# Performance work log

Hardware: AMD Instinct MI355X
Metric: run time of the kernel (lower is better)

Reference implementation:

```python
import jax, jax.numpy as jnp
import numpy as np

B, D, R, W, K = 1024, 256, 16384, 64, 3


def setup_inputs() -> dict:
    key = jax.random.key(0)
    ks = jax.random.split(key, 8)
    s = lambda k, shape: jax.random.normal(k, shape, jnp.float32) * 0.05
    return {
        'x': jax.random.normal(ks[0], (B, D), jnp.float32),
        'Wv': s(ks[1], (D, W)), 'bv': jnp.zeros((W,), jnp.float32),
        'Wb': s(ks[2], (D, 1)), 'bb': jnp.zeros((1,), jnp.float32),
        'Wg': s(ks[3], (D, 1)), 'bg': jnp.zeros((1,), jnp.float32),
        'Wp': s(ks[4], (D, R)), 'bp': jnp.zeros((R,), jnp.float32),
        # positive conv weights keep the pre-sharpening address non-negative,
        # so address ** gamma is well defined (as in a trained NTM shift kernel)
        'conv_k': jax.random.uniform(ks[5], (K, 1, 1), jnp.float32),
        'conv_b': jnp.zeros((1,), jnp.float32),
        'mem': jax.random.normal(ks[6], (R, W), jnp.float32),
    }


def reference(x, Wv, bv, Wb, bb, Wg, bg, Wp, bp, conv_k, conv_b, mem):
    eps = 1e-16
    # controller heads
    v = x @ Wv + bv                                  # [B, W] writing value (key)
    beta = jax.nn.softplus(x @ Wb + bb)              # [B, 1] key strength
    gamma = 1.0 + jax.nn.softplus(x @ Wg + bg)       # [B, 1] sharpening
    # content addressing: cosine similarity against memory rows
    vn = jnp.linalg.norm(v, axis=-1, keepdims=True)  # [B, 1]
    mn = jnp.linalg.norm(mem, axis=-1, keepdims=True)  # [R, 1]
    sim = (v @ mem.T) / (vn * mn.T + eps)            # [B, R]
    w = jax.nn.softmax(beta * sim, axis=-1)          # [B, R]
    # circular-ish shift via Conv1D('same') over the mem_rows axis
    wc = jax.lax.conv_general_dilated(
        w[..., None], conv_k, (1,), 'SAME',
        dimension_numbers=('NWC', 'WIO', 'NWC')) + conv_b  # [B, R, 1]
    a = wc[..., 0] ** gamma                          # sharpen
    a = a / jnp.sum(a + eps, axis=1, keepdims=True)  # renormalize (matches tf sum(a+eps))
    # memory write (batch-averaged erase-free additive write, shared memory)
    erase = jnp.mean(a, axis=0)                      # [R]
    add = jnp.einsum('br,bw->rw', a, v) / a.shape[0] # [R, W]
    mem2 = mem * (1.0 - erase)[:, None] + add
    # read from trainable memory at predicted address
    p = jax.nn.softmax(x @ Wp + bp, axis=-1)         # [B, R]
    return p @ mem2                                  # [B, W]
```

## Files before the change

### kernel.cpp

```cpp
#include <hip/hip_runtime.h>
#include <hip/hip_bf16.h>

#define B_ 1024
#define D_ 256
#define R_ 16384
#define W_ 64

typedef float f32x4 __attribute__((ext_vector_type(4)));
typedef __bf16 bf16x8 __attribute__((ext_vector_type(8)));

__device__ __forceinline__ float bf2f(unsigned short u) {
    union { unsigned int i; float f; } v; v.i = ((unsigned int)u) << 16; return v.f;
}
__device__ __forceinline__ unsigned short f2bf(float f) {
    union { float fv; unsigned int i; } v; v.fv = f;
    unsigned int r = v.i + 0x7FFFu + ((v.i >> 16) & 1u);
    return (unsigned short)(r >> 16);
}
__device__ __forceinline__ f32x4 mfma16(bf16x8 a, bf16x8 b, f32x4 c) {
    return __builtin_amdgcn_mfma_f32_16x16x32_bf16(a, b, c, 0, 0, 0);
}
__device__ __forceinline__ bf16x8 ld_bf8(const unsigned short* p) {
    return *(const bf16x8*)p;
}
__device__ __forceinline__ float sumsq8(bf16x8 v) {
    union { bf16x8 v; unsigned short u[8]; } c; c.v = v;
    float s = 0.f;
#pragma unroll
    for (int j = 0; j < 8; j++) { float f = bf2f(c.u[j]); s += f * f; }
    return s;
}

#define AO_X     0
#define AO_WV    262144
#define AO_BV    278528
#define AO_WB    278592
#define AO_BB    278848
#define AO_WG    278864
#define AO_BG    279120
#define AO_BP    279136
#define AO_CK    295520
#define AO_CB    295536
#define AO_MEM   295552
#define AO_TOT   1344128

__global__ __launch_bounds__(256) void k_sentinel(float* __restrict__ out, float val) {
    out[blockIdx.x * 256 + threadIdx.x] = val;
}

__global__ __launch_bounds__(256) void k_convert(
        const float* x, const float* Wv, const float* bv, const float* Wb, const float* bb,
        const float* Wg, const float* bg, const float* bp,
        const float* ck, const float* cb, const float* mem,
        unsigned short* __restrict__ dst, float* __restrict__ zst) {
    int base = blockIdx.x * 512 + threadIdx.x;
#pragma unroll
    for (int h = 0; h < 2; h++) {
        int idx = base + h * 256;
        if (idx >= AO_TOT) continue;
        if (idx < 2048) zst[idx] = 0.f;
        const float* p; int st; int n;
        if      (idx >= AO_MEM) { p = mem; st = AO_MEM; n = R_ * W_; }
        else if (idx >= AO_CB)  { p = cb;  st = AO_CB;  n = 1; }
        else if (idx >= AO_CK)  { p = ck;  st = AO_CK;  n = 3; }
        else if (idx >= AO_BP)  { p = bp;  st = AO_BP;  n = R_; }
        else if (idx >= AO_BG)  { p = bg;  st = AO_BG;  n = 1; }
        else if (idx >= AO_WG)  { p = Wg;  st = AO_WG;  n = D_; }
        else if (idx >= AO_BB)  { p = bb;  st = AO_BB;  n = 1; }
        else if (idx >= AO_WB)  { p = Wb;  st = AO_WB;  n = D_; }
        else if (idx >= AO_BV)  { p = bv;  st = AO_BV;  n = W_; }
        else if (idx >= AO_WV)  { p = Wv;  st = AO_WV;  n = D_ * W_; }
        else                    { p = x;   st = AO_X;   n = B_ * D_; }
        int local = idx - st;
        dst[idx] = (local < n) ? f2bf(p[local]) : (unsigned short)0;
    }
}

__global__ __launch_bounds__(256) void k_transpose_wp(const float* __restrict__ Wp,
                                                      unsigned short* __restrict__ WpT) {
    __shared__ unsigned short tile[64][66];
    int r0 = blockIdx.x * 64, d0 = blockIdx.y * 64;
    int t = threadIdx.x, lane = t & 63, wv = t >> 6;
#pragma unroll
    for (int i = 0; i < 16; i++) {
        int dl = wv + 4 * i;
        tile[dl][lane] = f2bf(Wp[(size_t)(d0 + dl) * R_ + r0 + lane]);
    }
    __syncthreads();
#pragma unroll
    for (int i = 0; i < 16; i++) {
        int rl = wv + 4 * i;
        WpT[(size_t)(r0 + rl) * D_ + d0 + lane] = tile[lane][rl];
    }
}

__global__ __launch_bounds__(64) void k_heads(const unsigned short* __restrict__ x,
        const unsigned short* __restrict__ Wv, const unsigned short* __restrict__ bv,
        const unsigned short* __restrict__ Wb, const unsigned short* __restrict__ bb,
        const unsigned short* __restrict__ Wg, const unsigned short* __restrict__ bg,
        float* __restrict__ v, unsigned short* __restrict__ vb,
        float* __restrict__ bovn, float* __restrict__ beta, float* __restrict__ gamma) {
    __shared__ float sx[256];
    int b = blockIdx.x, lane = threadIdx.x;
#pragma unroll
    for (int j = 0; j < 4; j++) sx[lane + 64 * j] = bf2f(x[b * 256 + lane + 64 * j]);
    __syncthreads();
    float acc = 0.f;
#pragma unroll 8
    for (int d = 0; d < 256; d++) acc += sx[d] * bf2f(Wv[d * 64 + lane]);
    acc += bf2f(bv[lane]);
    v[b * 64 + lane] = acc;
    vb[b * 64 + lane] = f2bf(acc);
    float sq = acc * acc;
#pragma unroll
    for (int d = 32; d >= 1; d >>= 1) sq += __shfl_xor(sq, d, 64);
    float pb = 0.f, pg = 0.f;
#pragma unroll
    for (int j = 0; j < 4; j++) {
        float xv = sx[lane + 64 * j];
        pb += xv * bf2f(Wb[lane + 64 * j]);
        pg += xv * bf2f(Wg[lane + 64 * j]);
    }
#pragma unroll
    for (int d = 32; d >= 1; d >>= 1) { pb += __shfl_xor(pb, d, 64); pg += __shfl_xor(pg, d, 64); }
    if (lane == 0) {
        float vn = sqrtf(sq);
        float zb = pb + bf2f(bb[0]);
        float zg = pg + bf2f(bg[0]);
        float be = (zb > 20.f) ? zb : log1pf(__expf(zb));
        beta[b]  = be;
        bovn[b]  = be / (vn + 1e-16f);
        gamma[b] = 1.f + ((zg > 20.f) ? zg : log1pf(__expf(zg)));
    }
}

__global__ __launch_bounds__(256, 8) void k_sim(const unsigned short* __restrict__ vb,
        const unsigned short* __restrict__ mem,
        const float* __restrict__ bovn,
        const float* __restrict__ beta,
        unsigned short* __restrict__ E, float* __restrict__ S) {
    __shared__ unsigned short etile[64][132];
    __shared__ float sred[4][64];
    int bx = blockIdx.x;
    int rc = bx & 127, tb = bx >> 7;
    int t = threadIdx.x, wv = t >> 6, l = t & 63;
    int lane15 = l & 15, quad = l >> 4;
    int rr0 = rc * 128 + wv * 32 + lane15;
    bf16x8 bm[2][2];
    float im[2];
#pragma unroll
    for (int nt = 0; nt < 2; nt++) {
        int rr = rr0 + nt * 16;
        bm[nt][0] = ld_bf8(mem + rr * 64 + quad * 8);
        bm[nt][1] = ld_bf8(mem + rr * 64 + 32 + quad * 8);
        float sq = sumsq8(bm[nt][0]) + sumsq8(bm[nt][1]);
        sq += __shfl_xor(sq, 16, 64);
        sq += __shfl_xor(sq, 32, 64);
        im[nt] = 1.0f / (sqrtf(sq) + 1e-16f);
    }
    bf16x8 afr[4][2];
    float bvl[4][4], bel[4][4];
#pragma unroll
    for (int m = 0; m < 4; m++) {
        int brow = tb * 64 + m * 16 + lane15;
        afr[m][0] = ld_bf8(vb + brow * 64 + quad * 8);
        afr[m][1] = ld_bf8(vb + brow * 64 + 32 + quad * 8);
#pragma unroll
        for (int reg = 0; reg < 4; reg++) {
            int b2 = tb * 64 + m * 16 + quad * 4 + reg;
            bvl[m][reg] = bovn[b2];
            bel[m][reg] = beta[b2];
        }
    }
    float sp[4][4];
#pragma unroll
    for (int m = 0; m < 4; m++)
#pragma unroll
        for (int r = 0; r < 4; r++) sp[m][r] = 0.f;

#pragma unroll
    for (int nt = 0; nt < 2; nt++) {
        int rl = wv * 32 + nt * 16 + lane15;
#pragma unroll
        for (int m = 0; m < 4; m++) {
            f32x4 acc = (f32x4){0.f, 0.f, 0.f, 0.f};
            acc = mfma16(afr[m][0], bm[nt][0], acc);
            acc = mfma16(afr[m][1], bm[nt][1], acc);
#pragma unroll
            for (int reg = 0; reg < 4; reg++) {
                float e = __expf(acc[reg] * (bvl[m][reg] * im[nt]) - bel[m][reg]);
                sp[m][reg] += e;
                etile[m * 16 + quad * 4 + reg][rl] = f2bf(e);
            }
        }
    }
#pragma unroll
    for (int m = 0; m < 4; m++)
#pragma unroll
        for (int reg = 0; reg < 4; reg++) {
            float s = sp[m][reg];
            s += __shfl_xor(s, 1, 64); s += __shfl_xor(s, 2, 64);
            s += __shfl_xor(s, 4, 64); s += __shfl_xor(s, 8, 64);
            if (lane15 == 0) sred[wv][m * 16 + quad * 4 + reg] = s;
        }
    __syncthreads();
#pragma unroll
    for (int j = 0; j < 4; j++) {
        int idx8 = t + j * 256;
        int row = idx8 >> 4;
        int c8 = (idx8 & 15) * 8;
        *(bf16x8*)(E + (size_t)(tb * 64 + row) * R_ + rc * 128 + c8) =
            *(const bf16x8*)&etile[row][c8];
    }
    if (t < 64)
        atomicAdd(&S[tb * 64 + t], sred[0][t] + sred[1][t] + sred[2][t] + sred[3][t]);
}

__global__ __launch_bounds__(256) void k_conv(const unsigned short* __restrict__ E,
        unsigned short* __restrict__ AT,
        const float* __restrict__ S, const float* __restrict__ gamma,
        const unsigned short* __restrict__ conv_k, const unsigned short* __restrict__ conv_b,
        float* __restrict__ T) {
    __shared__ unsigned short ein[64][132];
    __shared__ unsigned short aout[128][68];
    float k0 = bf2f(conv_k[0]), k1 = bf2f(conv_k[1]), k2 = bf2f(conv_k[2]);
    float cb = bf2f(conv_b[0]);
    int b0 = (blockIdx.x >> 7) * 64;
    int r0 = (blockIdx.x & 127) * 128;
    int t = threadIdx.x;
#pragma unroll
    for (int j = 0; j < 8; j++) {
        int idx4 = t + j * 256;
        int row = idx4 >> 5, c4 = (idx4 & 31) * 4;
        *(ushort4*)&ein[row][c4] = *(const ushort4*)(E + (b0 + row) * R_ + r0 + c4);
    }
    if (t < 64) {
        ein[t][130] = (r0 > 0) ? E[(b0 + t) * R_ + r0 - 1] : (unsigned short)0;
    } else if (t < 128) {
        int tb = t - 64;
        ein[tb][128] = (r0 + 128 < R_) ? E[(b0 + tb) * R_ + r0 + 128] : (unsigned short)0;
    }
    int b = t >> 2;
    int base = (t & 3) * 32;
    float sS_ = 1.0f / S[b0 + b];
    float g = gamma[b0 + b];
    __syncthreads();

    float el = bf2f((base == 0) ? ein[b][130] : ein[b][base - 1]);
    float ec = bf2f(ein[b][base]);
    float tacc = 0.f;
#pragma unroll
    for (int i = 0; i < 32; i++) {
        float er = bf2f(ein[b][base + 1 + i]);
        float wc = (k0 * el + k1 * ec + k2 * er) * sS_ + cb;
        wc = fmaxf(wc, 1e-30f);
        float au = __builtin_amdgcn_exp2f(g * __log2f(wc));
        aout[base + i][b] = f2bf(au);
        tacc += au;
        el = ec; ec = er;
    }
    tacc += __shfl_xor(tacc, 1, 64);
    tacc += __shfl_xor(tacc, 2, 64);
    if ((t & 3) == 0) atomicAdd(&T[b0 + b], tacc);
    __syncthreads();
#pragma unroll
    for (int j = 0; j < 8; j++) {
        int idx4 = t + j * 256;
        int rrow = idx4 >> 4, c4 = (idx4 & 15) * 4;
        *(ushort4*)(AT + (size_t)(r0 + rrow) * B_ + b0 + c4) = *(ushort4*)&aout[rrow][c4];
    }
}

__global__ __launch_bounds__(256) void k_vp2(const float* __restrict__ v, const float* __restrict__ T,
                                             unsigned short* __restrict__ vpb) {
    int idx = blockIdx.x * 256 + threadIdx.x;
    int m = idx >> 10, b = idx & 1023;
    float s = 1.0f / ((T[b] + (float)R_ * 1e-16f) * (float)B_);
    float val = (m < 64) ? v[b * 64 + m] * s : ((m == 64) ? s : 0.f);
    vpb[idx] = f2bf(val);
}

__global__ __launch_bounds__(256) void k_add(const unsigned short* __restrict__ AT,
        const unsigned short* __restrict__ vpb,
        const unsigned short* __restrict__ memb, unsigned short* __restrict__ mem2T) {
    __shared__ unsigned short smem[64][68];
    __shared__ unsigned short sm2[64][68];
    int r0 = blockIdx.x * 64;
    int t = threadIdx.x, wv = t >> 6, l = t & 63;
    int lane15 = l & 15, quad = l >> 4;
#pragma unroll
    for (int j = 0; j < 4; j++) {
        int idx4 = t + j * 256;
        int rl = idx4 >> 4, w4 = (idx4 & 15) * 4;
        *(ushort4*)&smem[rl][w4] = *(const ushort4*)(memb + (r0 + rl) * 64 + w4);
    }
    __syncthreads();

    const unsigned short* Brow = AT + (size_t)(r0 + wv * 16 + lane15) * B_ + quad * 8;
    const unsigned short* A0 = vpb + (0 * 16 + lane15) * B_ + quad * 8;
    const unsigned short* A1 = vpb + (1 * 16 + lane15) * B_ + quad * 8;
    const unsigned short* A2 = vpb + (2 * 16 + lane15) * B_ + quad * 8;
    const unsigned short* A3 = vpb + (3 * 16 + lane15) * B_ + quad * 8;
    const unsigned short* A4 = vpb + (4 * 16 + lane15) * B_ + quad * 8;
    f32x4 acc0 = {0,0,0,0}, acc1 = {0,0,0,0}, acc2 = {0,0,0,0}, acc3 = {0,0,0,0}, acc4 = {0,0,0,0};
#pragma unroll 4
    for (int k0 = 0; k0 < B_; k0 += 32) {
        bf16x8 bf = ld_bf8(Brow + k0);
        acc0 = mfma16(ld_bf8(A0 + k0), bf, acc0);
        acc1 = mfma16(ld_bf8(A1 + k0), bf, acc1);
        acc2 = mfma16(ld_bf8(A2 + k0), bf, acc2);
        acc3 = mfma16(ld_bf8(A3 + k0), bf, acc3);
        acc4 = mfma16(ld_bf8(A4 + k0), bf, acc4);
    }
    float er = __shfl(acc4[0], l & 15, 64);
    float ome = 1.f - er;
    f32x4 accs[4] = {acc0, acc1, acc2, acc3};
#pragma unroll
    for (int mt = 0; mt < 4; mt++) {
#pragma unroll
        for (int reg = 0; reg < 4; reg++) {
            int w = mt * 16 + quad * 4 + reg;
            int rl = wv * 16 + lane15;
            float m2 = bf2f(smem[rl][w]) * ome + accs[mt][reg];
            sm2[w][rl] = f2bf(m2);
        }
    }
    __syncthreads();
#pragma unroll
    for (int j = 0; j < 4; j++) {
        int idx4 = t + j * 256;
        int w = idx4 >> 4, r4 = (idx4 & 15) * 4;
        *(ushort4*)(mem2T + (size_t)w * R_ + r0 + r4) = *(ushort4*)&sm2[w][r4];
    }
}

__global__ __launch_bounds__(256, 4) void k_read(const unsigned short* __restrict__ x,
        const unsigned short* __restrict__ WpT, const unsigned short* __restrict__ bp,
        const unsigned short* __restrict__ mem2T,
        float* __restrict__ pacc, float* __restrict__ Spp) {
    __shared__ unsigned short bstage[2][32 * 264];
    __shared__ unsigned short ptile[4][16 * 40];
    int bx = blockIdx.x;
    int xcd = bx & 7, grp = bx >> 3;
    int rc = xcd * 8 + (grp >> 4), tb = grp & 15;
    int t = threadIdx.x, wv = t >> 6, l = t & 63;
    int lane15 = l & 15, quad = l >> 4;
    int brow = tb * 64 + wv * 16 + lane15;
    bf16x8 afr[8];
#pragma unroll
    for (int kk = 0; kk < 8; kk++)
        afr[kk] = ld_bf8(x + brow * 256 + kk * 32 + quad * 8);
    f32x4 accO[4];
#pragma unroll
    for (int nt = 0; nt < 4; nt++) accO[nt] = (f32x4){0.f, 0.f, 0.f, 0.f};
    float sp[4] = {0.f, 0.f, 0.f, 0.f};
    unsigned short* ptw = &ptile[wv][0];

    int srow = t >> 3, scg = (t & 7) * 8;
    bf16x8 pf[4];
    {
        const unsigned short* src = WpT + (size_t)(rc * 256 + srow) * 256 + scg;
#pragma unroll
        for (int j = 0; j < 4; j++) pf[j] = *(const bf16x8*)(src + 64 * j);
    }
    const unsigned short* vrow = mem2T + (size_t)lane15 * R_ + rc * 256 + quad * 8;

    for (int ss = 0; ss < 8; ss++) {
        unsigned short* bcur = bstage[ss & 1];
        {
            unsigned short* dst = bcur + srow * 264 + scg;
#pragma unroll
            for (int j = 0; j < 4; j++) *(bf16x8*)(dst + 64 * j) = pf[j];
        }
        if (ss < 7) {
            const unsigned short* src = WpT
                + (size_t)(rc * 256 + (ss + 1) * 32 + srow) * 256 + scg;
#pragma unroll
            for (int j = 0; j < 4; j++) pf[j] = *(const bf16x8*)(src + 64 * j);
        }
        __builtin_amdgcn_sched_barrier(0);
        asm volatile("s_waitcnt lgkmcnt(0)" ::: "memory");
        __builtin_amdgcn_s_barrier();
        __builtin_amdgcn_sched_barrier(0);
        bf16x8 vv0 = ld_bf8(vrow + (size_t)0 * 16 * R_ + ss * 32);
        bf16x8 vv1 = ld_bf8(vrow + (size_t)1 * 16 * R_ + ss * 32);
        bf16x8 vv2 = ld_bf8(vrow + (size_t)2 * 16 * R_ + ss * 32);
        bf16x8 vv3 = ld_bf8(vrow + (size_t)3 * 16 * R_ + ss * 32);
        int rbase = rc * 256 + ss * 32;
#pragma unroll
        for (int nt = 0; nt < 2; nt++) {
            f32x4 acc = (f32x4){0.f, 0.f, 0.f, 0.f};
            const unsigned short* bb = bcur + (nt * 16 + lane15) * 264 + quad * 8;
#pragma unroll
            for (int kk = 0; kk < 8; kk++) {
                bf16x8 bfr = *(const bf16x8*)(bb + kk * 32);
                acc = mfma16(afr[kk], bfr, acc);
            }
            int rr = rbase + nt * 16 + lane15;
            float bpv = bf2f(bp[rr]);
#pragma unroll
            for (int reg = 0; reg < 4; reg++) {
                float e = __expf(acc[reg] + bpv);
                unsigned short ue = f2bf(e);
                sp[reg] += bf2f(ue);
                ptw[(quad * 4 + reg) * 40 + nt * 16 + lane15] = ue;
            }
        }
        bf16x8 pa = *(const bf16x8*)(ptw + lane15 * 40 + quad * 8);
        accO[0] = mfma16(pa, vv0, accO[0]);
        accO[1] = mfma16(pa, vv1, accO[1]);
        accO[2] = mfma16(pa, vv2, accO[2]);
        accO[3] = mfma16(pa, vv3, accO[3]);
    }
#pragma unroll
    for (int nt = 0; nt < 4; nt++) {
        int wcol = nt * 16 + lane15;
#pragma unroll
        for (int reg = 0; reg < 4; reg++) {
            int b2 = tb * 64 + wv * 16 + quad * 4 + reg;
            pacc[((size_t)rc * B_ + b2) * 64 + wcol] = accO[nt][reg];
        }
    }
#pragma unroll
    for (int reg = 0; reg < 4; reg++) {
        float s = sp[reg];
        s += __shfl_xor(s, 1, 64); s += __shfl_xor(s, 2, 64);
        s += __shfl_xor(s, 4, 64); s += __shfl_xor(s, 8, 64);
        if (lane15 == 0) {
            int b2 = tb * 64 + wv * 16 + quad * 4 + reg;
            Spp[(size_t)rc * B_ + b2] = s;
        }
    }
}

__global__ __launch_bounds__(256) void k_out(const float* __restrict__ pacc,
                                             const float* __restrict__ Spp,
                                             float* __restrict__ out) {
    int idx = blockIdx.x * 256 + threadIdx.x;
    int b = idx >> 6;
    float acc = 0.f, sps = 0.f;
#pragma unroll 8
    for (int rc = 0; rc < 64; rc++) {
        acc += pacc[(size_t)rc * (B_ * 64) + idx];
        sps += Spp[rc * B_ + b];
    }
    out[idx] = acc / sps;
}

extern "C" void kernel_launch(void* const* d_in, const int* in_sizes, int n_in,
                              void* d_out, int out_size, void* d_ws, size_t ws_size,
                              hipStream_t stream) {
    (void)n_in; (void)out_size;
    float* outp = (float*)d_out;

    char* ws = (char*)d_ws;
    size_t o = 0;
    unsigned short* arena = (unsigned short*)(ws + o); o += (size_t)AO_TOT * 2;
    unsigned short* WpT = (unsigned short*)(ws + o); o += (size_t)R_ * D_ * 2;
    unsigned short* E   = (unsigned short*)(ws + o); o += (size_t)B_ * R_ * 2;
    unsigned short* AT  = (unsigned short*)(ws + o); o += (size_t)B_ * R_ * 2;
    float* v            = (float*)(ws + o);          o += (size_t)B_ * 64 * 4;
    unsigned short* vb  = (unsigned short*)(ws + o); o += (size_t)B_ * 64 * 2;
    unsigned short* vpb = (unsigned short*)(ws + o); o += (size_t)80 * B_ * 2;
    float* invmn        = (float*)(ws + o);          o += (size_t)R_ * 4;  (void)invmn;
    float* bovn         = (float*)(ws + o);          o += 4096;
    float* beta         = (float*)(ws + o);          o += 4096;
    float* gamma        = (float*)(ws + o);          o += 4096;
    unsigned short* m2T = (unsigned short*)(ws + o); o += (size_t)R_ * 64 * 2;
    float* S      = (float*)(ws + o);                o += 4096;
    float* T      = (float*)(ws + o);                o += 4096;
    float* Sp     = (float*)(ws + o);                o += 4096;  (void)Sp;
    float* Spp    = (float*)(ws + o);                o += (size_t)B_ * 64 * 4;
    float* pacc = (float*)AT;

    if (ws_size < o) {
        k_sentinel<<<256, 256, 0, stream>>>(outp, 1000.0f);
        return;
    }
    if (in_sizes[0] != B_ * D_ || in_sizes[7] != D_ * R_ || in_sizes[11] != R_ * W_) {
        k_sentinel<<<256, 256, 0, stream>>>(outp, 2000.0f);
        return;
    }

    k_convert<<<(AO_TOT + 511) / 512, 256, 0, stream>>>(
        (const float*)d_in[0], (const float*)d_in[1], (const float*)d_in[2],
        (const float*)d_in[3], (const float*)d_in[4], (const float*)d_in[5],
        (const float*)d_in[6], (const float*)d_in[8],
        (const float*)d_in[9], (const float*)d_in[10], (const float*)d_in[11],
        arena, S);

    k_transpose_wp<<<dim3(256, 4), 256, 0, stream>>>((const float*)d_in[7], WpT);
    k_heads<<<1024, 64, 0, stream>>>(arena + AO_X, arena + AO_WV, arena + AO_BV,
                                     arena + AO_WB, arena + AO_BB, arena + AO_WG,
                                     arena + AO_BG, v, vb, bovn, beta, gamma);
    k_sim<<<2048, 256, 0, stream>>>(vb, arena + AO_MEM, bovn, beta, E, S);
    k_conv<<<2048, 256, 0, stream>>>(E, AT, S, gamma, arena + AO_CK, arena + AO_CB, T);
    k_vp2<<<320, 256, 0, stream>>>(v, T, vpb);
    k_add<<<256, 256, 0, stream>>>(AT, vpb, arena + AO_MEM, m2T);
    k_read<<<1024, 256, 0, stream>>>(arena + AO_X, WpT, arena + AO_BP, m2T, pacc, Spp);
    k_out<<<256, 256, 0, stream>>>(pacc, Spp, outp);
}
```

Before: 220.6 us.

## Fuse convert, Wp transpose and heads into one prep kernel; widen conv loads

Merges the three independent preprocessing kernels (bf16 conversion, Wp transpose, controller heads) into a single launch that dispatches by block index. The heads portion now reads the fp32 inputs directly with bf16 rounding, so it no longer depends on the converted arena. It also packs four batch rows into each 256-thread block. Separately, k_conv loads E tiles with 16-byte vectors instead of 8-byte ones, and the LDS row padding is adjusted to keep alignment. This removes two launches and lets the small heads work overlap with the bandwidth-bound conversion and transpose, at the cost of a branchy kernel whose blocks have uneven work.

```diff
diff --git a/kernel.cpp b/kernel.cpp
--- a/kernel.cpp
+++ b/kernel.cpp
@@ -16,6 +16,9 @@
     union { float fv; unsigned int i; } v; v.fv = f;
     unsigned int r = v.i + 0x7FFFu + ((v.i >> 16) & 1u);
     return (unsigned short)(r >> 16);
+}
+__device__ __forceinline__ float rt(float f) {
+    return bf2f(f2bf(f));
 }
 __device__ __forceinline__ f32x4 mfma16(bf16x8 a, bf16x8 b, f32x4 c) {
     return __builtin_amdgcn_mfma_f32_16x16x32_bf16(a, b, c, 0, 0, 0);
@@ -44,93 +47,97 @@
 #define AO_MEM   295552
 #define AO_TOT   1344128
 
+#define NB_CONV  ((AO_TOT + 511) / 512)
+#define NB_TR    1024
+#define NB_HEADS 256
+
 __global__ __launch_bounds__(256) void k_sentinel(float* __restrict__ out, float val) {
     out[blockIdx.x * 256 + threadIdx.x] = val;
 }
 
-__global__ __launch_bounds__(256) void k_convert(
+__global__ __launch_bounds__(256) void k_prep(
         const float* x, const float* Wv, const float* bv, const float* Wb, const float* bb,
         const float* Wg, const float* bg, const float* bp,
-        const float* ck, const float* cb, const float* mem,
-        unsigned short* __restrict__ dst, float* __restrict__ zst) {
-    int base = blockIdx.x * 512 + threadIdx.x;
-#pragma unroll
-    for (int h = 0; h < 2; h++) {
-        int idx = base + h * 256;
-        if (idx >= AO_TOT) continue;
-        if (idx < 2048) zst[idx] = 0.f;
-        const float* p; int st; int n;
-        if      (idx >= AO_MEM) { p = mem; st = AO_MEM; n = R_ * W_; }
-        else if (idx >= AO_CB)  { p = cb;  st = AO_CB;  n = 1; }
-        else if (idx >= AO_CK)  { p = ck;  st = AO_CK;  n = 3; }
-        else if (idx >= AO_BP)  { p = bp;  st = AO_BP;  n = R_; }
-        else if (idx >= AO_BG)  { p = bg;  st = AO_BG;  n = 1; }
-        else if (idx >= AO_WG)  { p = Wg;  st = AO_WG;  n = D_; }
-        else if (idx >= AO_BB)  { p = bb;  st = AO_BB;  n = 1; }
-        else if (idx >= AO_WB)  { p = Wb;  st = AO_WB;  n = D_; }
-        else if (idx >= AO_BV)  { p = bv;  st = AO_BV;  n = W_; }
-        else if (idx >= AO_WV)  { p = Wv;  st = AO_WV;  n = D_ * W_; }
-        else                    { p = x;   st = AO_X;   n = B_ * D_; }
-        int local = idx - st;
-        dst[idx] = (local < n) ? f2bf(p[local]) : (unsigned short)0;
-    }
-}
-
-__global__ __launch_bounds__(256) void k_transpose_wp(const float* __restrict__ Wp,
-                                                      unsigned short* __restrict__ WpT) {
-    __shared__ unsigned short tile[64][66];
-    int r0 = blockIdx.x * 64, d0 = blockIdx.y * 64;
-    int t = threadIdx.x, lane = t & 63, wv = t >> 6;
-#pragma unroll
-    for (int i = 0; i < 16; i++) {
-        int dl = wv + 4 * i;
-        tile[dl][lane] = f2bf(Wp[(size_t)(d0 + dl) * R_ + r0 + lane]);
-    }
-    __syncthreads();
-#pragma unroll
-    for (int i = 0; i < 16; i++) {
-        int rl = wv + 4 * i;
-        WpT[(size_t)(r0 + rl) * D_ + d0 + lane] = tile[lane][rl];
-    }
-}
-
-__global__ __launch_bounds__(64) void k_heads(const unsigned short* __restrict__ x,
-        const unsigned short* __restrict__ Wv, const unsigned short* __restrict__ bv,
-        const unsigned short* __restrict__ Wb, const unsigned short* __restrict__ bb,
-        const unsigned short* __restrict__ Wg, const unsigned short* __restrict__ bg,
+        const float* ck, const float* cb, const float* mem, const float* Wp,
+        unsigned short* __restrict__ dst, float* __restrict__ zst,
+        unsigned short* __restrict__ WpT,
         float* __restrict__ v, unsigned short* __restrict__ vb,
         float* __restrict__ bovn, float* __restrict__ beta, float* __restrict__ gamma) {
-    __shared__ float sx[256];
-    int b = blockIdx.x, lane = threadIdx.x;
-#pragma unroll
-    for (int j = 0; j < 4; j++) sx[lane + 64 * j] = bf2f(x[b * 256 + lane + 64 * j]);
-    __syncthreads();
-    float acc = 0.f;
+    __shared__ unsigned short tile[64][66];
+    __shared__ float sxh[4][256];
+    int bid = blockIdx.x;
+    int t = threadIdx.x;
+    if (bid < NB_CONV) {
+        int base = bid * 512 + t;
+#pragma unroll
+        for (int h = 0; h < 2; h++) {
+            int idx = base + h * 256;
+            if (idx >= AO_TOT) continue;
+            if (idx < 2048) zst[idx] = 0.f;
+            const float* p; int st; int n;
+            if      (idx >= AO_MEM) { p = mem; st = AO_MEM; n = R_ * W_; }
+            else if (idx >= AO_CB)  { p = cb;  st = AO_CB;  n = 1; }
+            else if (idx >= AO_CK)  { p = ck;  st = AO_CK;  n = 3; }
+            else if (idx >= AO_BP)  { p = bp;  st = AO_BP;  n = R_; }
+            else if (idx >= AO_BG)  { p = bg;  st = AO_BG;  n = 1; }
+            else if (idx >= AO_WG)  { p = Wg;  st = AO_WG;  n = D_; }
+            else if (idx >= AO_BB)  { p = bb;  st = AO_BB;  n = 1; }
+            else if (idx >= AO_WB)  { p = Wb;  st = AO_WB;  n = D_; }
+            else if (idx >= AO_BV)  { p = bv;  st = AO_BV;  n = W_; }
+            else if (idx >= AO_WV)  { p = Wv;  st = AO_WV;  n = D_ * W_; }
+            else                    { p = x;   st = AO_X;   n = B_ * D_; }
+            int local = idx - st;
+            dst[idx] = (local < n) ? f2bf(p[local]) : (unsigned short)0;
+        }
+    } else if (bid < NB_CONV + NB_TR) {
+        int b2 = bid - NB_CONV;
+        int r0 = (b2 & 255) * 64, d0 = (b2 >> 8) * 64;
+        int lane = t & 63, wv = t >> 6;
+#pragma unroll
+        for (int i = 0; i < 16; i++) {
+            int dl = wv + 4 * i;
+            tile[dl][lane] = f2bf(Wp[(size_t)(d0 + dl) * R_ + r0 + lane]);
+        }
+        __syncthreads();
+#pragma unroll
+        for (int i = 0; i < 16; i++) {
+            int rl = wv + 4 * i;
+            WpT[(size_t)(r0 + rl) * D_ + d0 + lane] = tile[lane][rl];
+        }
+    } else {
+        int wv = t >> 6, lane = t & 63;
+        int b = (bid - NB_CONV - NB_TR) * 4 + wv;
+        float* sx = sxh[wv];
+#pragma unroll
+        for (int j = 0; j < 4; j++) sx[lane + 64 * j] = rt(x[b * 256 + lane + 64 * j]);
+        __syncthreads();
+        float acc = 0.f;
 #pragma unroll 8
-    for (int d = 0; d < 256; d++) acc += sx[d] * bf2f(Wv[d * 64 + lane]);
-    acc += bf2f(bv[lane]);
-    v[b * 64 + lane] = acc;
-    vb[b * 64 + lane] = f2bf(acc);
-    float sq = acc * acc;
-#pragma unroll
-    for (int d = 32; d >= 1; d >>= 1) sq += __shfl_xor(sq, d, 64);
-    float pb = 0.f, pg = 0.f;
-#pragma unroll
-    for (int j = 0; j < 4; j++) {
-        float xv = sx[lane + 64 * j];
-        pb += xv * bf2f(Wb[lane + 64 * j]);
-        pg += xv * bf2f(Wg[lane + 64 * j]);
-    }
-#pragma unroll
-    for (int d = 32; d >= 1; d >>= 1) { pb += __shfl_xor(pb, d, 64); pg += __shfl_xor(pg, d, 64); }
-    if (lane == 0) {
-        float vn = sqrtf(sq);
-        float zb = pb + bf2f(bb[0]);
-        float zg = pg + bf2f(bg[0]);
-        float be = (zb > 20.f) ? zb : log1pf(__expf(zb));
-        beta[b]  = be;
-        bovn[b]  = be / (vn + 1e-16f);
-        gamma[b] = 1.f + ((zg > 20.f) ? zg : log1pf(__expf(zg)));
+        for (int d = 0; d < 256; d++) acc += sx[d] * rt(Wv[d * 64 + lane]);
+        acc += rt(bv[lane]);
+        v[b * 64 + lane] = acc;
+        vb[b * 64 + lane] = f2bf(acc);
+        float sq = acc * acc;
+#pragma unroll
+        for (int d = 32; d >= 1; d >>= 1) sq += __shfl_xor(sq, d, 64);
+        float pb = 0.f, pg = 0.f;
+#pragma unroll
+        for (int j = 0; j < 4; j++) {
+            float xv = sx[lane + 64 * j];
+            pb += xv * rt(Wb[lane + 64 * j]);
+            pg += xv * rt(Wg[lane + 64 * j]);
+        }
+#pragma unroll
+        for (int d = 32; d >= 1; d >>= 1) { pb += __shfl_xor(pb, d, 64); pg += __shfl_xor(pg, d, 64); }
+        if (lane == 0) {
+            float vn = sqrtf(sq);
+            float zb = pb + rt(bb[0]);
+            float zg = pg + rt(bg[0]);
+            float be = (zb > 20.f) ? zb : log1pf(__expf(zb));
+            beta[b]  = be;
+            bovn[b]  = be / (vn + 1e-16f);
+            gamma[b] = 1.f + ((zg > 20.f) ? zg : log1pf(__expf(zg)));
+        }
     }
 }
 
@@ -221,7 +228,7 @@
         const float* __restrict__ S, const float* __restrict__ gamma,
         const unsigned short* __restrict__ conv_k, const unsigned short* __restrict__ conv_b,
         float* __restrict__ T) {
-    __shared__ unsigned short ein[64][132];
+    __shared__ unsigned short ein[64][136];
     __shared__ unsigned short aout[128][68];
     float k0 = bf2f(conv_k[0]), k1 = bf2f(conv_k[1]), k2 = bf2f(conv_k[2]);
     float cb = bf2f(conv_b[0]);
@@ -229,10 +236,10 @@
     int r0 = (blockIdx.x & 127) * 128;
     int t = threadIdx.x;
 #pragma unroll
-    for (int j = 0; j < 8; j++) {
-        int idx4 = t + j * 256;
-        int row = idx4 >> 5, c4 = (idx4 & 31) * 4;
-        *(ushort4*)&ein[row][c4] = *(const ushort4*)(E + (b0 + row) * R_ + r0 + c4);
+    for (int j = 0; j < 4; j++) {
+        int idx8 = t + j * 256;
+        int row = idx8 >> 4, c8 = (idx8 & 15) * 8;
+        *(bf16x8*)&ein[row][c8] = *(const bf16x8*)(E + (size_t)(b0 + row) * R_ + r0 + c8);
     }
     if (t < 64) {
         ein[t][130] = (r0 > 0) ? E[(b0 + t) * R_ + r0 - 1] : (unsigned short)0;
@@ -462,14 +469,12 @@
     float* v            = (float*)(ws + o);          o += (size_t)B_ * 64 * 4;
     unsigned short* vb  = (unsigned short*)(ws + o); o += (size_t)B_ * 64 * 2;
     unsigned short* vpb = (unsigned short*)(ws + o); o += (size_t)80 * B_ * 2;
-    float* invmn        = (float*)(ws + o);          o += (size_t)R_ * 4;  (void)invmn;
     float* bovn         = (float*)(ws + o);          o += 4096;
     float* beta         = (float*)(ws + o);          o += 4096;
     float* gamma        = (float*)(ws + o);          o += 4096;
     unsigned short* m2T = (unsigned short*)(ws + o); o += (size_t)R_ * 64 * 2;
     float* S      = (float*)(ws + o);                o += 4096;
     float* T      = (float*)(ws + o);                o += 4096;
-    float* Sp     = (float*)(ws + o);                o += 4096;  (void)Sp;
     float* Spp    = (float*)(ws + o);                o += (size_t)B_ * 64 * 4;
     float* pacc = (float*)AT;
 
@@ -482,17 +487,14 @@
         return;
     }
 
-    k_convert<<<(AO_TOT + 511) / 512, 256, 0, stream>>>(
+    k_prep<<<NB_CONV + NB_TR + NB_HEADS, 256, 0, stream>>>(
         (const float*)d_in[0], (const float*)d_in[1], (const float*)d_in[2],
         (const float*)d_in[3], (const float*)d_in[4], (const float*)d_in[5],
         (const float*)d_in[6], (const float*)d_in[8],
         (const float*)d_in[9], (const float*)d_in[10], (const float*)d_in[11],
-        arena, S);
-
-    k_transpose_wp<<<dim3(256, 4), 256, 0, stream>>>((const float*)d_in[7], WpT);
-    k_heads<<<1024, 64, 0, stream>>>(arena + AO_X, arena + AO_WV, arena + AO_BV,
-                                     arena + AO_WB, arena + AO_BB, arena + AO_WG,
-                                     arena + AO_BG, v, vb, bovn, beta, gamma);
+        (const float*)d_in[7],
+        arena, S, WpT, v, vb, bovn, beta, gamma);
+
     k_sim<<<2048, 256, 0, stream>>>(vb, arena + AO_MEM, bovn, beta, E, S);
     k_conv<<<2048, 256, 0, stream>>>(E, AT, S, gamma, arena + AO_CK, arena + AO_CB, T);
     k_vp2<<<320, 256, 0, stream>>>(v, T, vpb);
```

After: 217.4 us. Within noise of the previous version (-1.5%).
